# Optimization experiments

Measured on AMD Instinct MI355X. Metric: run time of the kernel, lower is better.

## Reference

```python
import jax, jax.numpy as jnp
import numpy as np

B, D, A, K, M = 32768, 64, 32, 16, 128


def _spec(W):
    # SpectralLinear: weight divided by its largest singular value
    s = jnp.linalg.norm(W, ord=2)
    return W / (s + 1e-6)


def setup_inputs() -> dict:
    key = jax.random.key(0)
    ks = jax.random.split(key, 20)

    def rn(i, shape):
        return jax.random.normal(ks[i], shape, jnp.float32) / np.float32(np.sqrt(shape[0]))

    return {
        "z": jax.random.normal(ks[0], (B, D), jnp.float32),
        "action": jax.random.normal(ks[1], (B, A), jnp.float32),
        "rw": jax.random.uniform(ks[2], (B, K), jnp.float32),
        "control": jax.random.normal(ks[3], (B, D), jnp.float32),
        # ActionTokenizer(action_dim, d_model, latent_dim) params (act / control / chart)
        "act_Wx": rn(4, (A + D, M)), "act_bx": jnp.zeros((M,), jnp.float32), "act_Wz": rn(5, (A, D)),
        "ctl_Wx": rn(6, (2 * D, M)), "ctl_bx": jnp.zeros((M,), jnp.float32), "ctl_Wz": rn(7, (D, D)),
        "cht_Wx": rn(8, (K + D, M)), "cht_bx": jnp.zeros((M,), jnp.float32), "cht_Wz": rn(9, (K, D)),
        # z_embed
        "We": rn(10, (D, M)), "be": jnp.zeros((M,), jnp.float32),
        # CovariantAttention (n_heads=1)
        "Wq": rn(11, (M, M)), "Wk": rn(12, (M, M)), "Wv": rn(13, (M, M)), "Wo": rn(14, (M, M)),
        # Spectral output heads
        "cons_W": rn(15, (M, 1)), "cons_b": jnp.zeros((1,), jnp.float32),
        "form_W": rn(16, (M, D)), "form_b": jnp.zeros((D,), jnp.float32),
    }


def reference(z, action, rw, control,
              act_Wx, act_bx, act_Wz,
              ctl_Wx, ctl_bx, ctl_Wz,
              cht_Wx, cht_bx, cht_Wz,
              We, be, Wq, Wk, Wv, Wo,
              cons_W, cons_b, form_W, form_b):
    def tok(u, Wx, bx, Wz):
        # tokenizer: feature token in d_model + associated latent position token
        x = jnp.tanh(jnp.concatenate([u, z], axis=-1) @ Wx + bx)   # [B, M]
        zt = z + jnp.tanh(u @ Wz)                                   # [B, D]
        return x, zt

    act_x, act_z = tok(action, act_Wx, act_bx, act_Wz)
    ctl_x, ctl_z = tok(control, ctl_Wx, ctl_bx, ctl_Wz)
    cht_x, cht_z = tok(rw, cht_Wx, cht_bx, cht_Wz)

    ctx_x = jnp.stack([act_x, ctl_x, cht_x], axis=1)  # [B, 3, M]
    ctx_z = jnp.stack([act_z, ctl_z, cht_z], axis=1)  # [B, 3, D]

    x_q = z @ We + be                                  # [B, M]

    # CovariantAttention: dot-product scores with metric-aware (geodesic distance) bias
    q = x_q @ Wq                                       # [B, M]
    k = ctx_x @ Wk                                     # [B, 3, M]
    v = ctx_x @ Wv                                     # [B, 3, M]
    dist2 = jnp.sum((z[:, None, :] - ctx_z) ** 2, axis=-1)          # [B, 3]
    scores = jnp.einsum('bm,btm->bt', q, k) / np.float32(np.sqrt(M)) - dist2
    attn = jax.nn.softmax(scores, axis=-1)             # [B, 3]
    feat = jnp.einsum('bt,btm->bm', attn, v) @ Wo      # [B, M]

    # Spectral output heads
    reward_conservative = feat @ _spec(cons_W) + cons_b            # [B, 1]
    reward_form_cov = feat @ _spec(form_W) + form_b                # [B, D]
    reward_nonconservative = jnp.sum(reward_form_cov * control, axis=-1, keepdims=True)

    return reward_conservative + reward_nonconservative            # [B, 1]
```

## Files before the change

kernel.cpp:

```cpp
#include <hip/hip_runtime.h>
#include <hip/hip_bf16.h>


typedef float f32x4 __attribute__((ext_vector_type(4)));
typedef short s16x8 __attribute__((ext_vector_type(8)));

#define OFF_ACTX  0
#define OFF_CTLX  24
#define OFF_CHTX  56
#define OFF_ACTZ  80
#define OFF_CTLZ  84
#define OFF_CHTZ  92
#define OFF_WEQK  96
#define OFF_WVOFT 112
#define N_TILES   128
#define SIG_OFF   (N_TILES*1024)
#define PREP_OFF  (SIG_OFF + 256)

__device__ __forceinline__ unsigned short f2bf(float f){
  unsigned u = __float_as_uint(f);
  u += 0x7fffu + ((u>>16)&1u);
  return (unsigned short)(u>>16);
}
__device__ __forceinline__ float ubf_lo(unsigned u){ return __uint_as_float(u<<16); }
__device__ __forceinline__ float ubf_hi(unsigned u){ return __uint_as_float(u & 0xffff0000u); }

union V8 { s16x8 v; unsigned short us[8]; uint4 q; };

__device__ __forceinline__ f32x4 MF(s16x8 a, s16x8 b, f32x4 c){
  return __builtin_amdgcn_mfma_f32_16x16x32_bf16(a, b, c, 0, 0, 0);
}

__device__ __forceinline__ s16x8 ldB(const unsigned short* pk, int tile, int lane){
  V8 t;
  t.q = *reinterpret_cast<const uint4*>(pk + ((tile<<6) + lane)*8);
  return t.v;
}

__device__ __forceinline__ s16x8 ldA_g(const float* __restrict__ p, int ko, int limit){
  V8 t;
  if (ko < limit){
    const float4* q4 = reinterpret_cast<const float4*>(p + ko);
    float4 a = q4[0], b = q4[1];
    t.us[0]=f2bf(a.x); t.us[1]=f2bf(a.y); t.us[2]=f2bf(a.z); t.us[3]=f2bf(a.w);
    t.us[4]=f2bf(b.x); t.us[5]=f2bf(b.y); t.us[6]=f2bf(b.z); t.us[7]=f2bf(b.w);
  } else {
    t.q = make_uint4(0u,0u,0u,0u);
  }
  return t.v;
}

__device__ __forceinline__ float tanh_fast(float x){
  x = fminf(15.f, fmaxf(-15.f, x));
  float e = __expf(2.f*x);
  return 1.f - __fdividef(2.f, e + 1.f);
}

__global__ __launch_bounds__(256) void prep_all(
    const float* __restrict__ We, const float* __restrict__ be,
    const float* __restrict__ Wq, const float* __restrict__ Wk,
    const float* __restrict__ Wv, const float* __restrict__ Wo,
    const float* __restrict__ consW, const float* __restrict__ formW,
    const float* __restrict__ aWx, const float* __restrict__ cWx,
    const float* __restrict__ hWx, const float* __restrict__ aWz,
    const float* __restrict__ cWz, const float* __restrict__ hWz,
    unsigned short* __restrict__ packed, float* __restrict__ prep,
    float* __restrict__ sig)
{
  const int b = blockIdx.x;
  const int tid = threadIdx.x;

  if (b < 130){
    __shared__ float Msh[128][129];
    __shared__ float tsh[128];
    if (b <= 64){
      for (int idx = tid; idx < 16384; idx += 256)
        Msh[idx >> 7][idx & 127] = Wk[idx];
      const float* rowv = (b == 64) ? be : (We + (size_t)b*128);
      if (tid < 128){
        float s = 0.f;
        for (int m = 0; m < 128; ++m) s += rowv[m]*Wq[(size_t)m*128 + tid];
        tsh[tid] = s;
      }
      __syncthreads();
      if (tid < 128){
        float s1 = 0.f;
        for (int p = 0; p < 128; ++p) s1 += tsh[p]*Msh[tid][p];
        if (b == 64) prep[16384 + tid] = s1;
        else {
          int r = b;
          int T = OFF_WEQK + ((r>>5)<<3) + (tid>>4);
          int l2 = (((r&31)>>3)<<4) | (tid&15);
          packed[((size_t)T*64 + l2)*8 + (r&7)] = f2bf(s1);
        }
      }
    } else {
      int d = b - 65;
      for (int idx = tid; idx < 16384; idx += 256)
        Msh[idx >> 7][idx & 127] = Wo[idx];
      __syncthreads();
      if (tid < 128){
        float s = 0.f;
        if (d < 64){ for (int j = 0; j < 128; ++j) s += Msh[tid][j]*formW[(size_t)j*64 + d]; }
        else       { for (int j = 0; j < 128; ++j) s += Msh[tid][j]*consW[j]; }
        tsh[tid] = s;
      }
      __syncthreads();
      for (int idx = tid; idx < 16384; idx += 256)
        Msh[idx >> 7][idx & 127] = Wv[idx];
      __syncthreads();
      if (tid < 128){
        float s1 = 0.f;
        for (int p = 0; p < 128; ++p) s1 += Msh[tid][p]*tsh[p];
        if (d < 64){
          int r = d;
          int T = OFF_WVOFT + ((r>>5)<<3) + (tid>>4);
          int l2 = (((r&31)>>3)<<4) | (tid&15);
          packed[((size_t)T*64 + l2)*8 + (r&7)] = f2bf(s1);
        } else prep[16512 + tid] = s1;
      }
    }
    return;
  }

  if (b == 130){
    __shared__ unsigned short SW[8192];
    __shared__ unsigned short SG[4096];

    #pragma unroll
    for (int s4 = 0; s4 < 4; ++s4){
      int q = tid*4 + s4;
      int T = q >> 6, l = q & 63;
      V8 t;
      #pragma unroll
      for (int i = 0; i < 8; ++i){
        int k = (T>>2)*32 + ((l>>4)<<3) + i;
        int n = ((T&3)<<4) + (l&15);
        t.us[i] = f2bf(formW[(size_t)k*64 + n]);
      }
      *reinterpret_cast<uint4*>(&SW[q*8]) = t.q;
    }
    __syncthreads();
    if (tid >= 64) return;
    const int l = tid;
    const f32x4 z4 = {0.f,0.f,0.f,0.f};

    float cs;
    { float c0 = consW[l], c1 = consW[l+64];
      cs = c0*c0 + c1*c1;
      #pragma unroll
      for (int m = 1; m < 64; m <<= 1) cs += __shfl_xor(cs, m);
    }

    s16x8 wf[4][4];
    #pragma unroll
    for (int kt = 0; kt < 4; ++kt)
      #pragma unroll
      for (int x = 0; x < 4; ++x)
        wf[kt][x] = *reinterpret_cast<const s16x8*>(&SW[((((kt<<2)+x)<<6) | l)*8]);

    f32x4 D[4][4];
    #pragma unroll
    for (int it = 0; it < 4; ++it)
      #pragma unroll
      for (int nt = 0; nt < 4; ++nt){
        f32x4 a = z4;
        #pragma unroll
        for (int kt = 0; kt < 4; ++kt) a = MF(wf[kt][it], wf[kt][nt], a);
        D[it][nt] = a;
      }

    float L;
    {
      float ss = 0.f;
      #pragma unroll
      for (int it = 0; it < 4; ++it)
        #pragma unroll
        for (int nt = 0; nt < 4; ++nt)
          #pragma unroll
          for (int j = 0; j < 4; ++j) ss += D[it][nt][j]*D[it][nt][j];
      #pragma unroll
      for (int m = 1; m < 64; m <<= 1) ss += __shfl_xor(ss, m);
      float n0 = sqrtf(ss);
      L = logf(n0);
      float iv = 1.f/n0;
      #pragma unroll
      for (int it = 0; it < 4; ++it){
        int rb  = it*16 + ((l>>4)<<2);
        int lp  = (((rb&31)>>3)<<4) | (l&15);
        int ib  = rb & 7;
        int ktg = rb >> 5;
        #pragma unroll
        for (int nt = 0; nt < 4; ++nt){
          unsigned w0 = (unsigned)f2bf(D[it][nt][0]*iv) | ((unsigned)f2bf(D[it][nt][1]*iv)<<16);
          unsigned w1 = (unsigned)f2bf(D[it][nt][2]*iv) | ((unsigned)f2bf(D[it][nt][3]*iv)<<16);
          uint2 u; u.x = w0; u.y = w1;
          *reinterpret_cast<uint2*>(&SG[((((ktg<<2)+nt)<<6 | lp))*8 + ib]) = u;
        }
      }
    }

    for (int s = 1; s <= 6; ++s){
      s16x8 gf[2][4];
      #pragma unroll
      for (int kt = 0; kt < 2; ++kt)
        #pragma unroll
        for (int x = 0; x < 4; ++x)
          gf[kt][x] = *reinterpret_cast<const s16x8*>(&SG[((((kt<<2)+x)<<6) | l)*8]);
      f32x4 E[4][4];
      #pragma unroll
      for (int it = 0; it < 4; ++it)
        #pragma unroll
        for (int nt = 0; nt < 4; ++nt){
          f32x4 a = MF(gf[0][it], gf[0][nt], z4);
          E[it][nt] = MF(gf[1][it], gf[1][nt], a);
        }
      float ss = 0.f;
      #pragma unroll
      for (int it = 0; it < 4; ++it)
        #pragma unroll
        for (int nt = 0; nt < 4; ++nt)
          #pragma unroll
          for (int j = 0; j < 4; ++j) ss += E[it][nt][j]*E[it][nt][j];
      #pragma unroll
      for (int m = 1; m < 64; m <<= 1) ss += __shfl_xor(ss, m);
      float ns = sqrtf(ss);
      L = 2.f*L + logf(ns);
      if (s < 6){
        float iv = 1.f/ns;
        #pragma unroll
        for (int it = 0; it < 4; ++it){
          int rb  = it*16 + ((l>>4)<<2);
          int lp  = (((rb&31)>>3)<<4) | (l&15);
          int ib  = rb & 7;
          int ktg = rb >> 5;
          #pragma unroll
          for (int nt = 0; nt < 4; ++nt){
            unsigned w0 = (unsigned)f2bf(E[it][nt][0]*iv) | ((unsigned)f2bf(E[it][nt][1]*iv)<<16);
            unsigned w1 = (unsigned)f2bf(E[it][nt][2]*iv) | ((unsigned)f2bf(E[it][nt][3]*iv)<<16);
            uint2 u; u.x = w0; u.y = w1;
            *reinterpret_cast<uint2*>(&SG[((((ktg<<2)+nt)<<6 | lp))*8 + ib]) = u;
          }
        }
      }
    }

    if (l == 0){
      float sf = expf(L*(1.f/128.f));
      sig[0] = 1.f/(sf + 1e-6f);
      sig[1] = 1.f/(sqrtf(cs) + 1e-6f);
    }
    return;
  }

  {
    int tile = b - 131;
    const float* W; int N; int kind = 0; int base;
    if      (tile < 24) { W=aWx; N=128; base=OFF_ACTX; }
    else if (tile < 56) { W=cWx; N=128; base=OFF_CTLX; }
    else if (tile < 80) { W=hWx; N=128; base=OFF_CHTX; kind=1; }
    else if (tile < 84) { W=aWz; N=64;  base=OFF_ACTZ; }
    else if (tile < 92) { W=cWz; N=64;  base=OFF_CTLZ; }
    else                { W=hWz; N=64;  base=OFF_CHTZ; kind=2; }
    int NT = N >> 4;
    int lt = tile - base;
    int nt = lt % NT, kt = lt / NT;
    int l = tid >> 2, i0 = (tid & 3)*2;
    unsigned short us2[2];
    #pragma unroll
    for (int di = 0; di < 2; ++di){
      int i = i0 + di;
      int k = kt*32 + ((l>>4)<<3) + i;
      int n = nt*16 + (l & 15);
      int sr = k;
      if (kind == 1) sr = (k < 16) ? k : (k < 32 ? -1 : k - 16);
      else if (kind == 2) sr = (k < 16) ? k : -1;
      float v = (sr >= 0) ? W[(size_t)sr*N + n] : 0.f;
      us2[di] = f2bf(v);
    }
    *reinterpret_cast<unsigned*>(&packed[((size_t)tile*64 + l)*8 + i0]) =
        (unsigned)us2[0] | ((unsigned)us2[1] << 16);
  }
}

template<int KTX, int KTZ>
__device__ __forceinline__ void token_reg(
    const unsigned short* pk, int offX, const s16x8* afX,
    int offZ, const s16x8* afZ, const float* __restrict__ bx,
    int lane, unsigned xp[8][2], float d2o[4])
{
  const int r15 = lane & 15;
  const f32x4 z4 = {0.f,0.f,0.f,0.f};
  f32x4 acc[8];
  #pragma unroll
  for (int nt = 0; nt < 8; ++nt) acc[nt] = z4;
  #pragma unroll
  for (int kt = 0; kt < KTX; ++kt){
    #pragma unroll
    for (int nt = 0; nt < 8; ++nt)
      acc[nt] = MF(afX[kt], ldB(pk, offX + kt*8 + nt, lane), acc[nt]);
  }
  #pragma unroll
  for (int nt = 0; nt < 8; ++nt){
    float bv = bx[nt*16 + r15];
    float v0 = tanh_fast(acc[nt][0] + bv);
    float v1 = tanh_fast(acc[nt][1] + bv);
    float v2 = tanh_fast(acc[nt][2] + bv);
    float v3 = tanh_fast(acc[nt][3] + bv);
    xp[nt][0] = (unsigned)f2bf(v0) | ((unsigned)f2bf(v1) << 16);
    xp[nt][1] = (unsigned)f2bf(v2) | ((unsigned)f2bf(v3) << 16);
  }
  f32x4 a2[4];
  #pragma unroll
  for (int nt = 0; nt < 4; ++nt) a2[nt] = z4;
  #pragma unroll
  for (int kt = 0; kt < KTZ; ++kt){
    #pragma unroll
    for (int nt = 0; nt < 4; ++nt)
      a2[nt] = MF(afZ[kt], ldB(pk, offZ + kt*4 + nt, lane), a2[nt]);
  }
  #pragma unroll
  for (int j = 0; j < 4; ++j){
    float s = 0.f;
    #pragma unroll
    for (int nt = 0; nt < 4; ++nt){ float t = tanh_fast(a2[nt][j]); s += t*t; }
    d2o[j] = s;
  }
  #pragma unroll
  for (int m = 1; m < 16; m <<= 1){
    #pragma unroll
    for (int j = 0; j < 4; ++j) d2o[j] += __shfl_xor(d2o[j], m);
  }
}

__global__ __launch_bounds__(512, 2) void reward_main(
    const float* __restrict__ z, const float* __restrict__ action,
    const float* __restrict__ rw, const float* __restrict__ control,
    const float* __restrict__ act_bx, const float* __restrict__ ctl_bx,
    const float* __restrict__ cht_bx, const float* __restrict__ consb,
    const float* __restrict__ formb,
    const unsigned short* __restrict__ packed, const float* __restrict__ prep,
    const float* __restrict__ sig, float* __restrict__ out)
{
  __shared__ unsigned short pk_sh[65536];

  const int tid  = threadIdx.x;
  const int wid  = tid >> 6;
  const int lane = tid & 63;
  const int g0   = blockIdx.x*128 + wid*16;
  const int r15  = lane & 15;
  const int hi   = lane >> 4;
  const int ko   = hi << 3;
  const int arow = g0 + r15;
  const f32x4 z4 = {0.f,0.f,0.f,0.f};

  {
    uint4* d4 = reinterpret_cast<uint4*>(pk_sh);
    const uint4* s4 = reinterpret_cast<const uint4*>(packed);
    #pragma unroll
    for (int it = 0; it < 16; ++it)
      d4[it*512 + tid] = s4[it*512 + tid];
  }
  __syncthreads();
  const unsigned short* pk = pk_sh;

  s16x8 fz0 = ldA_g(z + (size_t)arow*64,            ko, 64);
  s16x8 fz1 = ldA_g(z + (size_t)arow*64 + 32,       ko, 32);
  s16x8 fac = ldA_g(action + (size_t)arow*32,       ko, 32);
  s16x8 fc0 = ldA_g(control + (size_t)arow*64,      ko, 64);
  s16x8 fc1 = ldA_g(control + (size_t)arow*64 + 32, ko, 32);
  s16x8 frw = ldA_g(rw + (size_t)arow*16,           ko, 16);

  unsigned xpk[3][8][2];
  float d2[3][4];
  {
    s16x8 afA[3] = {fac, fz0, fz1};
    token_reg<3,1>(pk, OFF_ACTX, afA, OFF_ACTZ, &fac, act_bx, lane, xpk[0], d2[0]);
  }
  {
    s16x8 afC[4] = {fc0, fc1, fz0, fz1};
    s16x8 afCz[2] = {fc0, fc1};
    token_reg<4,2>(pk, OFF_CTLX, afC, OFF_CTLZ, afCz, ctl_bx, lane, xpk[1], d2[1]);
  }
  {
    s16x8 afH[3] = {frw, fz0, fz1};
    token_reg<3,1>(pk, OFF_CHTX, afH, OFF_CHTZ, &frw, cht_bx, lane, xpk[2], d2[2]);
  }

  f32x4 qw[8];
  {
    #pragma unroll
    for (int nt = 0; nt < 8; ++nt) qw[nt] = z4;
    s16x8 afE[2] = {fz0, fz1};
    #pragma unroll
    for (int kt = 0; kt < 2; ++kt)
      #pragma unroll
      for (int nt = 0; nt < 8; ++nt)
        qw[nt] = MF(afE[kt], ldB(pk, OFF_WEQK + kt*8 + nt, lane), qw[nt]);
    const float* bqk = prep + 16384;
    #pragma unroll
    for (int nt = 0; nt < 8; ++nt){
      float bv = bqk[nt*16 + r15];
      #pragma unroll
      for (int j = 0; j < 4; ++j) qw[nt][j] += bv;
    }
  }

  f32x4 g[8];
  {
    #pragma unroll
    for (int nt = 0; nt < 8; ++nt) g[nt] = z4;
    s16x8 afG[2] = {fc0, fc1};
    #pragma unroll
    for (int kt = 0; kt < 2; ++kt)
      #pragma unroll
      for (int nt = 0; nt < 8; ++nt)
        g[nt] = MF(afG[kt], ldB(pk, OFF_WVOFT + kt*8 + nt, lane), g[nt]);
  }

  float sp[3][4];
  #pragma unroll
  for (int t = 0; t < 3; ++t){
    #pragma unroll
    for (int j = 0; j < 4; ++j) sp[t][j] = 0.f;
    #pragma unroll
    for (int nt = 0; nt < 8; ++nt){
      unsigned p0 = xpk[t][nt][0], p1 = xpk[t][nt][1];
      sp[t][0] += ubf_lo(p0)*qw[nt][0];
      sp[t][1] += ubf_hi(p0)*qw[nt][1];
      sp[t][2] += ubf_lo(p1)*qw[nt][2];
      sp[t][3] += ubf_hi(p1)*qw[nt][3];
    }
  }
  #pragma unroll
  for (int m = 1; m < 16; m <<= 1)
    #pragma unroll
    for (int t = 0; t < 3; ++t)
      #pragma unroll
      for (int j = 0; j < 4; ++j) sp[t][j] += __shfl_xor(sp[t][j], m);

  float at[3][4];
  #pragma unroll
  for (int j = 0; j < 4; ++j){
    const float isq = 0.0883883476483184f;
    float s0 = sp[0][j]*isq - d2[0][j];
    float s1 = sp[1][j]*isq - d2[1][j];
    float s2 = sp[2][j]*isq - d2[2][j];
    float mx = fmaxf(s0, fmaxf(s1, s2));
    float e0 = __expf(s0 - mx), e1 = __expf(s1 - mx), e2 = __expf(s2 - mx);
    float inv = 1.f/(e0 + e1 + e2);
    at[0][j] = e0*inv; at[1][j] = e1*inv; at[2][j] = e2*inv;
  }

  float xb[8][4];
  #pragma unroll
  for (int nt = 0; nt < 8; ++nt){
    #pragma unroll
    for (int j = 0; j < 4; ++j){
      unsigned p = xpk[0][nt][j>>1];
      float v = at[0][j] * ((j&1) ? ubf_hi(p) : ubf_lo(p));
      p = xpk[1][nt][j>>1];
      v += at[1][j] * ((j&1) ? ubf_hi(p) : ubf_lo(p));
      p = xpk[2][nt][j>>1];
      v += at[2][j] * ((j&1) ? ubf_hi(p) : ubf_lo(p));
      xb[nt][j] = v;
    }
  }

  const float inv_f = sig[0], inv_c = sig[1], cb = consb[0];
  const float* wvoc = prep + 16512;
  float wv[8];
  #pragma unroll
  for (int nt = 0; nt < 8; ++nt) wv[nt] = wvoc[nt*16 + r15];

  float tot[4];
  #pragma unroll
  for (int j = 0; j < 4; ++j){
    float sc = 0.f, sg = 0.f;
    #pragma unroll
    for (int nt = 0; nt < 8; ++nt){
      sc += xb[nt][j]*wv[nt];
      sg += xb[nt][j]*g[nt][j];
    }
    tot[j] = inv_c*sc + inv_f*sg;
  }
  #pragma unroll
  for (int m = 1; m < 16; m <<= 1)
    #pragma unroll
    for (int j = 0; j < 4; ++j) tot[j] += __shfl_xor(tot[j], m);

  float fbp = 0.f;
  {
    const float* cp = control + (size_t)arow*64;
    float4 c0a = *(const float4*)(cp + ko);
    float4 c0b = *(const float4*)(cp + ko + 4);
    float4 c1a = *(const float4*)(cp + 32 + ko);
    float4 c1b = *(const float4*)(cp + 32 + ko + 4);
    float4 f0a = *(const float4*)(formb + ko);
    float4 f0b = *(const float4*)(formb + ko + 4);
    float4 f1a = *(const float4*)(formb + 32 + ko);
    float4 f1b = *(const float4*)(formb + 32 + ko + 4);
    fbp = c0a.x*f0a.x + c0a.y*f0a.y + c0a.z*f0a.z + c0a.w*f0a.w
        + c0b.x*f0b.x + c0b.y*f0b.y + c0b.z*f0b.z + c0b.w*f0b.w
        + c1a.x*f1a.x + c1a.y*f1a.y + c1a.z*f1a.z + c1a.w*f1a.w
        + c1b.x*f1b.x + c1b.y*f1b.y + c1b.z*f1b.z + c1b.w*f1b.w;
  }
  fbp += __shfl_xor(fbp, 16);
  fbp += __shfl_xor(fbp, 32);

  float fbj[4];
  #pragma unroll
  for (int j = 0; j < 4; ++j) fbj[j] = __shfl(fbp, hi*4 + j);
  if (r15 == 0){
    #pragma unroll
    for (int j = 0; j < 4; ++j) out[g0 + hi*4 + j] = tot[j] + fbj[j] + cb;
  }
}

extern "C" void kernel_launch(void* const* d_in, const int* in_sizes, int n_in,
                              void* d_out, int out_size, void* d_ws, size_t ws_size,
                              hipStream_t stream)
{
  const float* z      = (const float*)d_in[0];
  const float* action = (const float*)d_in[1];
  const float* rw     = (const float*)d_in[2];
  const float* control= (const float*)d_in[3];
  const float* actWx  = (const float*)d_in[4];
  const float* actbx  = (const float*)d_in[5];
  const float* actWz  = (const float*)d_in[6];
  const float* ctlWx  = (const float*)d_in[7];
  const float* ctlbx  = (const float*)d_in[8];
  const float* ctlWz  = (const float*)d_in[9];
  const float* chtWx  = (const float*)d_in[10];
  const float* chtbx  = (const float*)d_in[11];
  const float* chtWz  = (const float*)d_in[12];
  const float* We     = (const float*)d_in[13];
  const float* be     = (const float*)d_in[14];
  const float* Wq     = (const float*)d_in[15];
  const float* Wk     = (const float*)d_in[16];
  const float* Wv     = (const float*)d_in[17];
  const float* Wo     = (const float*)d_in[18];
  const float* consW  = (const float*)d_in[19];
  const float* consb  = (const float*)d_in[20];
  const float* formW  = (const float*)d_in[21];
  const float* formb  = (const float*)d_in[22];
  float* out = (float*)d_out;

  unsigned short* packed = (unsigned short*)d_ws;
  float* sig  = (float*)((char*)d_ws + SIG_OFF);
  float* prep = (float*)((char*)d_ws + PREP_OFF);

  hipLaunchKernelGGL(prep_all, dim3(227), dim3(256), 0, stream,
                     We, be, Wq, Wk, Wv, Wo, consW, formW,
                     actWx, ctlWx, chtWx, actWz, ctlWz, chtWz,
                     packed, prep, sig);
  hipLaunchKernelGGL(reward_main, dim3(256), dim3(512), 0, stream,
                     z, action, rw, control, actbx, ctlbx, chtbx,
                     consb, formb, packed, prep, sig, out);
}
```

Baseline: 41.21 us.

## Split output columns across two wave halves with shared-memory partial-sum exchange

Doubles the block to 1024 threads and gives each pair of waves the same 16 rows, with each wave handling half of the 128-wide feature columns and half of the latent columns. Partial attention scores, distance terms and final dot products are exchanged through small shared arrays, with two extra block barriers. The aim is more waves per CU to hide latency and to cut per-wave register use. The trade-off is the added synchronisation. A tighter launch-bounds hint may also force register spilling.

Result: no change. 41.78 us (+1.4%).

```diff
diff --git a/kernel.cpp b/kernel.cpp
--- a/kernel.cpp
+++ b/kernel.cpp
@@ -284,46 +284,46 @@
 }
 
 template<int KTX, int KTZ>
-__device__ __forceinline__ void token_reg(
+__device__ __forceinline__ void token_half(
     const unsigned short* pk, int offX, const s16x8* afX,
     int offZ, const s16x8* afZ, const float* __restrict__ bx,
-    int lane, unsigned xp[8][2], float d2o[4])
+    int lane, int ntb, int nzb, unsigned xp[4][2], float d2o[4])
 {
   const int r15 = lane & 15;
   const f32x4 z4 = {0.f,0.f,0.f,0.f};
-  f32x4 acc[8];
-  #pragma unroll
-  for (int nt = 0; nt < 8; ++nt) acc[nt] = z4;
+  f32x4 acc[4];
+  #pragma unroll
+  for (int nl = 0; nl < 4; ++nl) acc[nl] = z4;
   #pragma unroll
   for (int kt = 0; kt < KTX; ++kt){
     #pragma unroll
-    for (int nt = 0; nt < 8; ++nt)
-      acc[nt] = MF(afX[kt], ldB(pk, offX + kt*8 + nt, lane), acc[nt]);
-  }
-  #pragma unroll
-  for (int nt = 0; nt < 8; ++nt){
-    float bv = bx[nt*16 + r15];
-    float v0 = tanh_fast(acc[nt][0] + bv);
-    float v1 = tanh_fast(acc[nt][1] + bv);
-    float v2 = tanh_fast(acc[nt][2] + bv);
-    float v3 = tanh_fast(acc[nt][3] + bv);
-    xp[nt][0] = (unsigned)f2bf(v0) | ((unsigned)f2bf(v1) << 16);
-    xp[nt][1] = (unsigned)f2bf(v2) | ((unsigned)f2bf(v3) << 16);
-  }
-  f32x4 a2[4];
-  #pragma unroll
-  for (int nt = 0; nt < 4; ++nt) a2[nt] = z4;
+    for (int nl = 0; nl < 4; ++nl)
+      acc[nl] = MF(afX[kt], ldB(pk, offX + kt*8 + ntb + nl, lane), acc[nl]);
+  }
+  #pragma unroll
+  for (int nl = 0; nl < 4; ++nl){
+    float bv = bx[(ntb + nl)*16 + r15];
+    float v0 = tanh_fast(acc[nl][0] + bv);
+    float v1 = tanh_fast(acc[nl][1] + bv);
+    float v2 = tanh_fast(acc[nl][2] + bv);
+    float v3 = tanh_fast(acc[nl][3] + bv);
+    xp[nl][0] = (unsigned)f2bf(v0) | ((unsigned)f2bf(v1) << 16);
+    xp[nl][1] = (unsigned)f2bf(v2) | ((unsigned)f2bf(v3) << 16);
+  }
+  f32x4 a2[2];
+  #pragma unroll
+  for (int nl = 0; nl < 2; ++nl) a2[nl] = z4;
   #pragma unroll
   for (int kt = 0; kt < KTZ; ++kt){
     #pragma unroll
-    for (int nt = 0; nt < 4; ++nt)
-      a2[nt] = MF(afZ[kt], ldB(pk, offZ + kt*4 + nt, lane), a2[nt]);
+    for (int nl = 0; nl < 2; ++nl)
+      a2[nl] = MF(afZ[kt], ldB(pk, offZ + kt*4 + nzb + nl, lane), a2[nl]);
   }
   #pragma unroll
   for (int j = 0; j < 4; ++j){
     float s = 0.f;
     #pragma unroll
-    for (int nt = 0; nt < 4; ++nt){ float t = tanh_fast(a2[nt][j]); s += t*t; }
+    for (int nl = 0; nl < 2; ++nl){ float t = tanh_fast(a2[nl][j]); s += t*t; }
     d2o[j] = s;
   }
   #pragma unroll
@@ -333,7 +333,7 @@
   }
 }
 
-__global__ __launch_bounds__(512, 2) void reward_main(
+__global__ __launch_bounds__(1024, 4) void reward_main(
     const float* __restrict__ z, const float* __restrict__ action,
     const float* __restrict__ rw, const float* __restrict__ control,
     const float* __restrict__ act_bx, const float* __restrict__ ctl_bx,
@@ -343,23 +343,31 @@
     const float* __restrict__ sig, float* __restrict__ out)
 {
   __shared__ unsigned short pk_sh[65536];
+  __shared__ float exSp[8][2][3][16];
+  __shared__ float exD2[8][2][3][16];
+  __shared__ float exTot[8][2][16];
 
   const int tid  = threadIdx.x;
   const int wid  = tid >> 6;
   const int lane = tid & 63;
-  const int g0   = blockIdx.x*128 + wid*16;
+  const int rg   = wid & 7;
+  const int mh   = wid >> 3;
+  const int g0   = blockIdx.x*128 + rg*16;
   const int r15  = lane & 15;
   const int hi   = lane >> 4;
   const int ko   = hi << 3;
+  const int rb   = hi << 2;
   const int arow = g0 + r15;
+  const int ntb  = mh << 2;
+  const int nzb  = mh << 1;
   const f32x4 z4 = {0.f,0.f,0.f,0.f};
 
   {
     uint4* d4 = reinterpret_cast<uint4*>(pk_sh);
     const uint4* s4 = reinterpret_cast<const uint4*>(packed);
     #pragma unroll
-    for (int it = 0; it < 16; ++it)
-      d4[it*512 + tid] = s4[it*512 + tid];
+    for (int it = 0; it < 8; ++it)
+      d4[it*1024 + tid] = s4[it*1024 + tid];
   }
   __syncthreads();
   const unsigned short* pk = pk_sh;
@@ -371,51 +379,39 @@
   s16x8 fc1 = ldA_g(control + (size_t)arow*64 + 32, ko, 32);
   s16x8 frw = ldA_g(rw + (size_t)arow*16,           ko, 16);
 
-  unsigned xpk[3][8][2];
+  unsigned xpk[3][4][2];
   float d2[3][4];
   {
     s16x8 afA[3] = {fac, fz0, fz1};
-    token_reg<3,1>(pk, OFF_ACTX, afA, OFF_ACTZ, &fac, act_bx, lane, xpk[0], d2[0]);
+    token_half<3,1>(pk, OFF_ACTX, afA, OFF_ACTZ, &fac, act_bx, lane, ntb, nzb, xpk[0], d2[0]);
   }
   {
     s16x8 afC[4] = {fc0, fc1, fz0, fz1};
     s16x8 afCz[2] = {fc0, fc1};
-    token_reg<4,2>(pk, OFF_CTLX, afC, OFF_CTLZ, afCz, ctl_bx, lane, xpk[1], d2[1]);
+    token_half<4,2>(pk, OFF_CTLX, afC, OFF_CTLZ, afCz, ctl_bx, lane, ntb, nzb, xpk[1], d2[1]);
   }
   {
     s16x8 afH[3] = {frw, fz0, fz1};
-    token_reg<3,1>(pk, OFF_CHTX, afH, OFF_CHTZ, &frw, cht_bx, lane, xpk[2], d2[2]);
-  }
-
-  f32x4 qw[8];
-  {
-    #pragma unroll
-    for (int nt = 0; nt < 8; ++nt) qw[nt] = z4;
+    token_half<3,1>(pk, OFF_CHTX, afH, OFF_CHTZ, &frw, cht_bx, lane, ntb, nzb, xpk[2], d2[2]);
+  }
+
+  f32x4 qw[4];
+  {
+    #pragma unroll
+    for (int nl = 0; nl < 4; ++nl) qw[nl] = z4;
     s16x8 afE[2] = {fz0, fz1};
     #pragma unroll
     for (int kt = 0; kt < 2; ++kt)
       #pragma unroll
-      for (int nt = 0; nt < 8; ++nt)
-        qw[nt] = MF(afE[kt], ldB(pk, OFF_WEQK + kt*8 + nt, lane), qw[nt]);
+      for (int nl = 0; nl < 4; ++nl)
+        qw[nl] = MF(afE[kt], ldB(pk, OFF_WEQK + kt*8 + ntb + nl, lane), qw[nl]);
     const float* bqk = prep + 16384;
     #pragma unroll
-    for (int nt = 0; nt < 8; ++nt){
-      float bv = bqk[nt*16 + r15];
-      #pragma unroll
-      for (int j = 0; j < 4; ++j) qw[nt][j] += bv;
-    }
-  }
-
-  f32x4 g[8];
-  {
-    #pragma unroll
-    for (int nt = 0; nt < 8; ++nt) g[nt] = z4;
-    s16x8 afG[2] = {fc0, fc1};
-    #pragma unroll
-    for (int kt = 0; kt < 2; ++kt)
-      #pragma unroll
-      for (int nt = 0; nt < 8; ++nt)
-        g[nt] = MF(afG[kt], ldB(pk, OFF_WVOFT + kt*8 + nt, lane), g[nt]);
+    for (int nl = 0; nl < 4; ++nl){
+      float bv = bqk[(ntb + nl)*16 + r15];
+      #pragma unroll
+      for (int j = 0; j < 4; ++j) qw[nl][j] += bv;
+    }
   }
 
   float sp[3][4];
@@ -424,12 +420,12 @@
     #pragma unroll
     for (int j = 0; j < 4; ++j) sp[t][j] = 0.f;
     #pragma unroll
-    for (int nt = 0; nt < 8; ++nt){
-      unsigned p0 = xpk[t][nt][0], p1 = xpk[t][nt][1];
-      sp[t][0] += ubf_lo(p0)*qw[nt][0];
-      sp[t][1] += ubf_hi(p0)*qw[nt][1];
-      sp[t][2] += ubf_lo(p1)*qw[nt][2];
-      sp[t][3] += ubf_hi(p1)*qw[nt][3];
+    for (int nl = 0; nl < 4; ++nl){
+      unsigned p0 = xpk[t][nl][0], p1 = xpk[t][nl][1];
+      sp[t][0] += ubf_lo(p0)*qw[nl][0];
+      sp[t][1] += ubf_hi(p0)*qw[nl][1];
+      sp[t][2] += ubf_lo(p1)*qw[nl][2];
+      sp[t][3] += ubf_hi(p1)*qw[nl][3];
     }
   }
   #pragma unroll
@@ -438,49 +434,73 @@
     for (int t = 0; t < 3; ++t)
       #pragma unroll
       for (int j = 0; j < 4; ++j) sp[t][j] += __shfl_xor(sp[t][j], m);
+
+  if (r15 == 0){
+    #pragma unroll
+    for (int t = 0; t < 3; ++t)
+      #pragma unroll
+      for (int j = 0; j < 4; ++j){
+        exSp[rg][mh][t][rb+j] = sp[t][j];
+        exD2[rg][mh][t][rb+j] = d2[t][j];
+      }
+  }
+  __syncthreads();
 
   float at[3][4];
   #pragma unroll
   for (int j = 0; j < 4; ++j){
     const float isq = 0.0883883476483184f;
-    float s0 = sp[0][j]*isq - d2[0][j];
-    float s1 = sp[1][j]*isq - d2[1][j];
-    float s2 = sp[2][j]*isq - d2[2][j];
+    int r = rb + j;
+    float s0 = (exSp[rg][0][0][r] + exSp[rg][1][0][r])*isq - (exD2[rg][0][0][r] + exD2[rg][1][0][r]);
+    float s1 = (exSp[rg][0][1][r] + exSp[rg][1][1][r])*isq - (exD2[rg][0][1][r] + exD2[rg][1][1][r]);
+    float s2 = (exSp[rg][0][2][r] + exSp[rg][1][2][r])*isq - (exD2[rg][0][2][r] + exD2[rg][1][2][r]);
     float mx = fmaxf(s0, fmaxf(s1, s2));
     float e0 = __expf(s0 - mx), e1 = __expf(s1 - mx), e2 = __expf(s2 - mx);
     float inv = 1.f/(e0 + e1 + e2);
     at[0][j] = e0*inv; at[1][j] = e1*inv; at[2][j] = e2*inv;
   }
 
-  float xb[8][4];
-  #pragma unroll
-  for (int nt = 0; nt < 8; ++nt){
+  float xb[4][4];
+  #pragma unroll
+  for (int nl = 0; nl < 4; ++nl){
     #pragma unroll
     for (int j = 0; j < 4; ++j){
-      unsigned p = xpk[0][nt][j>>1];
+      unsigned p = xpk[0][nl][j>>1];
       float v = at[0][j] * ((j&1) ? ubf_hi(p) : ubf_lo(p));
-      p = xpk[1][nt][j>>1];
+      p = xpk[1][nl][j>>1];
       v += at[1][j] * ((j&1) ? ubf_hi(p) : ubf_lo(p));
-      p = xpk[2][nt][j>>1];
+      p = xpk[2][nl][j>>1];
       v += at[2][j] * ((j&1) ? ubf_hi(p) : ubf_lo(p));
-      xb[nt][j] = v;
-    }
+      xb[nl][j] = v;
+    }
+  }
+
+  f32x4 g[4];
+  {
+    #pragma unroll
+    for (int nl = 0; nl < 4; ++nl) g[nl] = z4;
+    s16x8 afG[2] = {fc0, fc1};
+    #pragma unroll
+    for (int kt = 0; kt < 2; ++kt)
+      #pragma unroll
+      for (int nl = 0; nl < 4; ++nl)
+        g[nl] = MF(afG[kt], ldB(pk, OFF_WVOFT + kt*8 + ntb + nl, lane), g[nl]);
   }
 
   const float inv_f = sig[0], inv_c = sig[1], cb = consb[0];
   const float* wvoc = prep + 16512;
-  float wv[8];
-  #pragma unroll
-  for (int nt = 0; nt < 8; ++nt) wv[nt] = wvoc[nt*16 + r15];
+  float wv[4];
+  #pragma unroll
+  for (int nl = 0; nl < 4; ++nl) wv[nl] = wvoc[(ntb + nl)*16 + r15];
 
   float tot[4];
   #pragma unroll
   for (int j = 0; j < 4; ++j){
     float sc = 0.f, sg = 0.f;
     #pragma unroll
-    for (int nt = 0; nt < 8; ++nt){
-      sc += xb[nt][j]*wv[nt];
-      sg += xb[nt][j]*g[nt][j];
+    for (int nl = 0; nl < 4; ++nl){
+      sc += xb[nl][j]*wv[nl];
+      sg += xb[nl][j]*g[nl][j];
     }
     tot[j] = inv_c*sc + inv_f*sg;
   }
@@ -489,31 +509,42 @@
     #pragma unroll
     for (int j = 0; j < 4; ++j) tot[j] += __shfl_xor(tot[j], m);
 
-  float fbp = 0.f;
-  {
-    const float* cp = control + (size_t)arow*64;
-    float4 c0a = *(const float4*)(cp + ko);
-    float4 c0b = *(const float4*)(cp + ko + 4);
-    float4 c1a = *(const float4*)(cp + 32 + ko);
-    float4 c1b = *(const float4*)(cp + 32 + ko + 4);
-    float4 f0a = *(const float4*)(formb + ko);
-    float4 f0b = *(const float4*)(formb + ko + 4);
-    float4 f1a = *(const float4*)(formb + 32 + ko);
-    float4 f1b = *(const float4*)(formb + 32 + ko + 4);
-    fbp = c0a.x*f0a.x + c0a.y*f0a.y + c0a.z*f0a.z + c0a.w*f0a.w
-        + c0b.x*f0b.x + c0b.y*f0b.y + c0b.z*f0b.z + c0b.w*f0b.w
-        + c1a.x*f1a.x + c1a.y*f1a.y + c1a.z*f1a.z + c1a.w*f1a.w
-        + c1b.x*f1b.x + c1b.y*f1b.y + c1b.z*f1b.z + c1b.w*f1b.w;
-  }
-  fbp += __shfl_xor(fbp, 16);
-  fbp += __shfl_xor(fbp, 32);
-
-  float fbj[4];
-  #pragma unroll
-  for (int j = 0; j < 4; ++j) fbj[j] = __shfl(fbp, hi*4 + j);
   if (r15 == 0){
     #pragma unroll
-    for (int j = 0; j < 4; ++j) out[g0 + hi*4 + j] = tot[j] + fbj[j] + cb;
+    for (int j = 0; j < 4; ++j) exTot[rg][mh][rb+j] = tot[j];
+  }
+  __syncthreads();
+
+  if (mh == 0){
+    float fbp = 0.f;
+    {
+      const float* cp = control + (size_t)arow*64;
+      float4 c0a = *(const float4*)(cp + ko);
+      float4 c0b = *(const float4*)(cp + ko + 4);
+      float4 c1a = *(const float4*)(cp + 32 + ko);
+      float4 c1b = *(const float4*)(cp + 32 + ko + 4);
+      float4 f0a = *(const float4*)(formb + ko);
+      float4 f0b = *(const float4*)(formb + ko + 4);
+      float4 f1a = *(const float4*)(formb + 32 + ko);
+      float4 f1b = *(const float4*)(formb + 32 + ko + 4);
+      fbp = c0a.x*f0a.x + c0a.y*f0a.y + c0a.z*f0a.z + c0a.w*f0a.w
+          + c0b.x*f0b.x + c0b.y*f0b.y + c0b.z*f0b.z + c0b.w*f0b.w
+          + c1a.x*f1a.x + c1a.y*f1a.y + c1a.z*f1a.z + c1a.w*f1a.w
+          + c1b.x*f1b.x + c1b.y*f1b.y + c1b.z*f1b.z + c1b.w*f1b.w;
+    }
+    fbp += __shfl_xor(fbp, 16);
+    fbp += __shfl_xor(fbp, 32);
+
+    float fbj[4];
+    #pragma unroll
+    for (int j = 0; j < 4; ++j) fbj[j] = __shfl(fbp, hi*4 + j);
+    if (r15 == 0){
+      #pragma unroll
+      for (int j = 0; j < 4; ++j){
+        int r = rb + j;
+        out[g0 + r] = exTot[rg][0][r] + exTot[rg][1][r] + fbj[j] + cb;
+      }
+    }
   }
 }
 
@@ -554,7 +585,7 @@
                      We, be, Wq, Wk, Wv, Wo, consW, formW,
                      actWx, ctlWx, chtWx, actWz, ctlWz, chtWz,
                      packed, prep, sig);
-  hipLaunchKernelGGL(reward_main, dim3(256), dim3(512), 0, stream,
+  hipLaunchKernelGGL(reward_main, dim3(256), dim3(1024), 0, stream,
                      z, action, rw, control, actbx, ctlbx, chtbx,
                      consb, formb, packed, prep, sig, out);
 }
```
